# Kernel tuning notes

Hardware: AMD Instinct MI355X
Metric: run time of the kernel (lower is better)

Reference implementation:

```python
import jax, jax.numpy as jnp
import numpy as np

HIDDEN = 512
D = 2 * HIDDEN  # 1024


def setup_inputs() -> dict:
    key = jax.random.key(0)
    ks = jax.random.split(key, 7)
    B, S = 8, 2048
    scale = 1.0 / np.sqrt(D)
    return {
        "lstm_out": jax.random.normal(ks[0], (B, S, D), dtype=jnp.float32),
        "Wq": jax.random.normal(ks[1], (D, D), dtype=jnp.float32) * scale,
        "bq": jnp.zeros((D,), dtype=jnp.float32),
        "Wk": jax.random.normal(ks[2], (D, D), dtype=jnp.float32) * scale,
        "bk": jnp.zeros((D,), dtype=jnp.float32),
        "Wv": jax.random.normal(ks[3], (D, D), dtype=jnp.float32) * scale,
        "bv": jnp.zeros((D,), dtype=jnp.float32),
    }


def reference(lstm_out, Wq, bq, Wk, bk, Wv, bv):
    # Q, K, V: [B, S, D]
    Q = jnp.einsum("bsd,de->bse", lstm_out, Wq) + bq
    K = jnp.einsum("bsd,de->bse", lstm_out, Wk) + bk
    V = jnp.einsum("bsd,de->bse", lstm_out, Wv) + bv
    # NOTE: original module has no 1/sqrt(d) scaling
    scores = jnp.einsum("bqd,bkd->bqk", Q, K)  # [B, S, S]
    weights = jax.nn.softmax(scores, axis=-1)
    context = jnp.einsum("bqk,bkd->bqd", weights, V)  # [B, S, D]
    return context
```

## Files before the change

### kernel.cpp

```cpp
#include <hip/hip_runtime.h>
#include <hip/hip_bf16.h>

static constexpr int S = 2048;
static constexpr int D = 1024;
static constexpr int NB = 8;

#define LOG2E 1.4426950408889634f

typedef float    f32x4  __attribute__((ext_vector_type(4)));
typedef _Float16 f16x4  __attribute__((ext_vector_type(4)));
typedef _Float16 f16x8  __attribute__((ext_vector_type(8)));

#define CM_F32    0
#define CM_TRANSV 2
#define CM_F16    3

#define GLD16(g, l) __builtin_amdgcn_global_load_lds(                         \
    (const __attribute__((address_space(1))) void*)(g),                       \
    (__attribute__((address_space(3))) void*)(l), 16, 0, 0)

#define MFMA16(a, b, c) __builtin_amdgcn_mfma_f32_16x16x32_f16((a), (b), (c), 0, 0, 0)
#define BAR() __builtin_amdgcn_s_barrier()
#define PRIO1() __builtin_amdgcn_s_setprio(1)
#define PRIO0() __builtin_amdgcn_s_setprio(0)
#define WAIT_LGKM(n) asm volatile("s_waitcnt lgkmcnt(" #n ")" ::: "memory")
#define WAIT_VM(n)   asm volatile("s_waitcnt vmcnt(" #n ")" ::: "memory")

template <int CMODE, int BNT>
__global__ __launch_bounds__(512, 1) void bgemm256(
    const _Float16* __restrict__ Ah_, long sAz,
    const _Float16* __restrict__ Bh_, long sBz,
    int lda, int ldb,
    void* __restrict__ C1, int ldc, long sCz,
    const float* __restrict__ bias, int K)
{
    extern __shared__ char smem[];
    constexpr int NW_N  = BNT / 64;
    constexpr int NW_M  = 8 / NW_N;
    constexpr int WM    = 256 / NW_M;
    constexpr int MI    = WM / 16;
    constexpr int APLANE = 16384;
    constexpr int BPLANE = BNT * 64;
    constexpr int BOFF   = 2 * APLANE;
    constexpr int BUFSZ  = 2 * APLANE + 2 * BPLANE;

    int bx, by, bz;
    {
        const int gx = gridDim.x, gy = gridDim.y;
        const int nwg = gx * gy * gridDim.z;
        const int wg = blockIdx.x + gx * (blockIdx.y + gy * blockIdx.z);
        const int q = nwg >> 3, r = nwg & 7;
        const int xcd = wg & 7, i = wg >> 3;
        const int nid = (xcd < r) ? xcd * (q + 1) + i
                                  : r * (q + 1) + (xcd - r) * q + i;
        bx = nid % gx;
        const int tmp = nid / gx;
        by = tmp % gy;
        bz = tmp / gy;
    }

    const int t = threadIdx.x;
    const int z = bz;
    const int m0 = by * 256;
    const int n0 = bx * BNT;
    const int lane = t & 63, wid = t >> 6;
    const int wr = wid / NW_N, wc = wid % NW_N;
    const int fr = lane & 15, fq = lane >> 4;
    const int lrow = lane >> 2, lslot = lane & 3;

    const _Float16* Ahz = Ah_ + (long)z * sAz;
    const _Float16* Bhz = Bh_ + (long)z * sBz;

    auto stA = [&](int tile, int p) {
        char* lbase = smem + (tile & 1) * BUFSZ + p * APLANE;
#pragma unroll
        for (int i = 0; i < 2; ++i) {
            const int row = wid * 32 + i * 16 + lrow;
            const int chunk = lslot ^ ((row >> 1) & 3);
            const long kk = (long)tile * 64 + p * 32 + chunk * 8;
            GLD16(Ahz + (long)(m0 + row) * lda + kk,
                  lbase + (wid * 32 + i * 16) * 64);
        }
    };
    auto stB = [&](int tile, int p) {
        char* lbase = smem + (tile & 1) * BUFSZ + BOFF + p * BPLANE;
        if constexpr (BNT == 256) {
#pragma unroll
            for (int i = 0; i < 2; ++i) {
                const int row = wid * 32 + i * 16 + lrow;
                const int chunk = lslot ^ ((row >> 1) & 3);
                const long kk = (long)tile * 64 + p * 32 + chunk * 8;
                GLD16(Bhz + (long)(n0 + row) * ldb + kk,
                      lbase + (wid * 32 + i * 16) * 64);
            }
        } else {
            const int row = wid * 16 + lrow;
            const int chunk = lslot ^ ((row >> 1) & 3);
            const long kk = (long)tile * 64 + p * 32 + chunk * 8;
            GLD16(Bhz + (long)(n0 + row) * ldb + kk, lbase + (wid * 16) * 64);
        }
    };
    auto rdA = [&](int buf, int p, int mi) -> f16x8 {
        const int row = wr * WM + mi * 16 + fr;
        const int slot = fq ^ ((row >> 1) & 3);
        return *(const f16x8*)(smem + buf * BUFSZ + p * APLANE +
                               row * 64 + slot * 16);
    };
    auto rdB = [&](int buf, int p, int ni) -> f16x8 {
        const int row = wc * 64 + ni * 16 + fr;
        const int slot = fq ^ ((row >> 1) & 3);
        return *(const f16x8*)(smem + buf * BUFSZ + BOFF + p * BPLANE +
                               row * 64 + slot * 16);
    };

    f32x4 acc[MI][4] = {};
    const int ktiles = K / 64;

    {
        f16x8 b0[4], b1[4], a0[MI], a1[MI];
        auto mb = [&](f16x8 (&A)[MI], f16x8 (&B)[4]) {
#pragma unroll
            for (int mi = 0; mi < MI; ++mi)
#pragma unroll
                for (int ni = 0; ni < 4; ++ni)
                    acc[mi][ni] = MFMA16(A[mi], B[ni], acc[mi][ni]);
        };
        stA(0, 0); stB(0, 0); stA(0, 1); stB(0, 1);
        WAIT_VM(0);
        BAR();
#pragma unroll
        for (int ni = 0; ni < 4; ++ni) b0[ni] = rdB(0, 0, ni);
#pragma unroll
        for (int mi = 0; mi < MI; ++mi) a0[mi] = rdA(0, 0, mi);

        for (int tt = 0; tt < ktiles; ++tt) {
            const int buf = tt & 1;
            const bool pf = (tt + 1 < ktiles);
            if (pf) {
                stA(tt + 1, 0); stB(tt + 1, 0);
                if constexpr (BNT == 256) WAIT_VM(4); else WAIT_VM(3);
            } else {
                WAIT_VM(0);
            }
            BAR();
#pragma unroll
            for (int ni = 0; ni < 4; ++ni) b1[ni] = rdB(buf, 1, ni);
#pragma unroll
            for (int mi = 0; mi < MI; ++mi) a1[mi] = rdA(buf, 1, mi);
            if constexpr (BNT == 256) WAIT_LGKM(12); else WAIT_LGKM(8);
            PRIO1(); mb(a0, b0); PRIO0();
            BAR();
            if (pf) {
                stA(tt + 1, 1); stB(tt + 1, 1);
                if constexpr (BNT == 256) WAIT_VM(4); else WAIT_VM(3);
            }
            WAIT_LGKM(0);
            BAR();
            PRIO1(); mb(a1, b1); PRIO0();
            if (pf) {
                const int nb = buf ^ 1;
#pragma unroll
                for (int ni = 0; ni < 4; ++ni) b0[ni] = rdB(nb, 0, ni);
#pragma unroll
                for (int mi = 0; mi < MI; ++mi) a0[mi] = rdA(nb, 0, mi);
            }
        }
    }

    if constexpr (CMODE == CM_TRANSV) {
        constexpr int LDT = 544;
#pragma unroll
        for (int mi = 0; mi < MI; ++mi) {
            const int row0 = wr * WM + mi * 16 + fq * 4;
#pragma unroll
            for (int ni = 0; ni < 4; ++ni) {
                const int colp = wc * 64 + ni * 16 + fr;
                const float bv = bias[n0 + colp];
                f16x4 h;
#pragma unroll
                for (int j = 0; j < 4; ++j) h[j] = (_Float16)(acc[mi][ni][j] + bv);
                *(f16x4*)(smem + colp * LDT + row0 * 2) = h;
            }
        }
        BAR();
        const int b_ = m0 >> 11;
        const int sbase = m0 & (S - 1);
        const int l31 = lane & 31, lh = lane >> 5;
        _Float16* Vp = (_Float16*)C1;
#pragma unroll
        for (int it = 0; it < 8; ++it) {
            const int dd = wid * 16 + it * 2 + lh;
            const f16x8 v = *(const f16x8*)(smem + dd * LDT + l31 * 16);
            *(f16x8*)(Vp + ((long)(b_ * D + n0 + dd)) * S + sbase + l31 * 8) = v;
        }
    } else {
#pragma unroll
        for (int mi = 0; mi < MI; ++mi) {
            const int rbase = m0 + wr * WM + mi * 16 + fq * 4;
#pragma unroll
            for (int ni = 0; ni < 4; ++ni) {
                const int col = n0 + wc * 64 + ni * 16 + fr;
                f32x4 a = acc[mi][ni];
                if (CMODE != CM_F32) {
                    const float bv = bias[col];
#pragma unroll
                    for (int j = 0; j < 4; ++j) a[j] += bv;
                }
                if (CMODE == CM_F32) {
                    float* C = (float*)C1 + (long)z * sCz;
#pragma unroll
                    for (int j = 0; j < 4; ++j)
                        C[(long)(rbase + j) * ldc + col] = a[j];
                } else {
                    _Float16* Ch = (_Float16*)C1;
#pragma unroll
                    for (int j = 0; j < 4; ++j)
                        Ch[(long)(rbase + j) * ldc + col] = (_Float16)a[j];
                }
            }
        }
    }
}

__global__ __launch_bounds__(256) void xsplit(
    const float* __restrict__ X, _Float16* __restrict__ Xh)
{
    const long i = ((long)blockIdx.x * 256 + threadIdx.x) * 8;
    f32x4 v0 = *(const f32x4*)(X + i);
    f32x4 v1 = *(const f32x4*)(X + i + 4);
    f16x8 h;
#pragma unroll
    for (int j = 0; j < 4; ++j) { h[j] = (_Float16)v0[j]; h[4 + j] = (_Float16)v1[j]; }
    *(f16x8*)(Xh + i) = h;
}

__global__ void wsplit(const float* __restrict__ W0, const float* __restrict__ W1,
                       const float* __restrict__ W2, _Float16* __restrict__ Th)
{
    const float* W = blockIdx.z == 0 ? W0 : (blockIdx.z == 1 ? W1 : W2);
    _Float16* th = Th + (long)blockIdx.z * 1024 * 1024;
    __shared__ float tile[32][33];
    const int bx = blockIdx.x * 32, by = blockIdx.y * 32;
    const int tx = threadIdx.x, ty = threadIdx.y;
#pragma unroll
    for (int i = ty; i < 32; i += 8) tile[i][tx] = W[(long)(by + i) * 1024 + bx + tx];
    __syncthreads();
#pragma unroll
    for (int i = ty; i < 32; i += 8)
        th[(long)(bx + i) * 1024 + by + tx] = (_Float16)tile[tx][i];
}

__global__ __launch_bounds__(256) void pconv(float* __restrict__ Sb)
{
    const long row = blockIdx.x;
    float* p = Sb + row * (long)S;
    const int t = threadIdx.x;

    f32x4 x0 = *(const f32x4*)(p + t * 8);
    f32x4 x1 = *(const f32x4*)(p + t * 8 + 4);

    float m = -3.4e38f;
#pragma unroll
    for (int j = 0; j < 4; ++j) m = fmaxf(m, fmaxf(x0[j], x1[j]));
#pragma unroll
    for (int o = 32; o >= 1; o >>= 1) m = fmaxf(m, __shfl_xor(m, o));

    __shared__ float wm[4], wsum[4];
    const int wid = t >> 6, lane = t & 63;
    if (lane == 0) wm[wid] = m;
    __syncthreads();
    m = fmaxf(fmaxf(wm[0], wm[1]), fmaxf(wm[2], wm[3]));

    float e[8], ssum = 0.f;
#pragma unroll
    for (int j = 0; j < 4; ++j) {
        e[j]     = exp2f((x0[j] - m) * LOG2E);
        e[4 + j] = exp2f((x1[j] - m) * LOG2E);
        ssum += e[j] + e[4 + j];
    }
#pragma unroll
    for (int o = 32; o >= 1; o >>= 1) ssum += __shfl_xor(ssum, o);
    if (lane == 0) wsum[wid] = ssum;
    __syncthreads();
    const float invl = 1.0f / (wsum[0] + wsum[1] + wsum[2] + wsum[3]);

    f16x8 outv;
#pragma unroll
    for (int j = 0; j < 8; ++j) outv[j] = (_Float16)(e[j] * invl);
    *(f16x8*)((_Float16*)p + t * 8) = outv;
}

extern "C" void kernel_launch(void* const* d_in, const int* in_sizes, int n_in,
                              void* d_out, int out_size, void* d_ws, size_t ws_size,
                              hipStream_t stream)
{
    const float* X  = (const float*)d_in[0];
    const float* Wq = (const float*)d_in[1];
    const float* bq = (const float*)d_in[2];
    const float* Wk = (const float*)d_in[3];
    const float* bk = (const float*)d_in[4];
    const float* Wv = (const float*)d_in[5];
    const float* bv = (const float*)d_in[6];
    float* out = (float*)d_out;
    char* ws = (char*)d_ws;
    const size_t MB = 1u << 20;

    _Float16* Wh = (_Float16*)ws;
    _Float16* Qh = (_Float16*)(ws + 6 * MB);
    _Float16* Kh = (_Float16*)(ws + 38 * MB);
    _Float16* Vt = (_Float16*)(ws + 70 * MB);
    float*    Sb = (float*)(ws + 102 * MB);
    _Float16* Xh = (_Float16*)(ws + 102 * MB);

    const int LDS_256 = 131072;
    const int LDS_128 = 98304;
    (void)hipFuncSetAttribute(reinterpret_cast<const void*>(&bgemm256<CM_F16, 256>),
                        hipFuncAttributeMaxDynamicSharedMemorySize, LDS_256);
    (void)hipFuncSetAttribute(reinterpret_cast<const void*>(&bgemm256<CM_F32, 256>),
                        hipFuncAttributeMaxDynamicSharedMemorySize, LDS_256);
    (void)hipFuncSetAttribute(reinterpret_cast<const void*>(&bgemm256<CM_TRANSV, 128>),
                        hipFuncAttributeMaxDynamicSharedMemorySize, LDS_128);

    xsplit<<<dim3(8192), 256, 0, stream>>>(X, Xh);
    wsplit<<<dim3(32, 32, 3), dim3(32, 8), 0, stream>>>(Wq, Wk, Wv, Wh);

    const long MW = 1024 * 1024;
    bgemm256<CM_F16, 256><<<dim3(D / 256, 64, 1), 512, LDS_256, stream>>>(
        Xh, 0, Wh, 0, D, D, Qh, D, 0, bq, D);
    bgemm256<CM_F16, 256><<<dim3(D / 256, 64, 1), 512, LDS_256, stream>>>(
        Xh, 0, Wh + MW, 0, D, D, Kh, D, 0, bk, D);
    bgemm256<CM_TRANSV, 128><<<dim3(D / 128, 64, 1), 512, LDS_128, stream>>>(
        Xh, 0, Wh + 2 * MW, 0, D, D, Vt, 0, 0, bv, D);

    bgemm256<CM_F32, 256><<<dim3(S / 256, S / 256, NB), 512, LDS_256, stream>>>(
        Qh, (long)S * D, Kh, (long)S * D,
        D, D, Sb, S, (long)S * S, nullptr, D);
    pconv<<<dim3(NB * S), 256, 0, stream>>>(Sb);
    bgemm256<CM_F32, 256><<<dim3(D / 256, S / 256, NB), 512, LDS_256, stream>>>(
        (const _Float16*)Sb, 2L * S * S, Vt, (long)D * S,
        2 * S, S, out, D, (long)S * D, nullptr, S);
}
```

Before: 324.6 us.

## Split BNT=256 GEMM main loop into four interleaved MFMA/load phases

For the 256-wide tile variant, the k-loop now runs four half-tile MFMA phases instead of two full ones. Global-to-LDS stores and LDS fragment reads are spread between these phases, so memory traffic overlaps more with matrix math and fewer fragments are live at once. The other tile variant only has its constexpr branches simplified. The finer schedule relies on tightly tuned wait counts and adds barrier and priority toggles that could cost more than they hide.

```diff
diff --git a/kernel.cpp b/kernel.cpp
--- a/kernel.cpp
+++ b/kernel.cpp
@@ -116,7 +116,78 @@
     f32x4 acc[MI][4] = {};
     const int ktiles = K / 64;
 
-    {
+    if constexpr (BNT == 256) {
+        f16x8 b0[4], b1[4], a0[8], a1[8];
+        stA(0, 0); stB(0, 0); stA(0, 1); stB(0, 1);
+        WAIT_VM(0);
+        BAR();
+#pragma unroll
+        for (int ni = 0; ni < 4; ++ni) b0[ni] = rdB(0, 0, ni);
+#pragma unroll
+        for (int mi = 0; mi < 4; ++mi) a0[mi] = rdA(0, 0, mi);
+
+        for (int tt = 0; tt < ktiles; ++tt) {
+            const int buf = tt & 1;
+            const bool pf = (tt + 1 < ktiles);
+            if (pf) stA(tt + 1, 0);
+#pragma unroll
+            for (int mi = 0; mi < 4; ++mi) a0[4 + mi] = rdA(buf, 0, 4 + mi);
+            WAIT_LGKM(4);
+            PRIO1();
+#pragma unroll
+            for (int mi = 0; mi < 4; ++mi)
+#pragma unroll
+                for (int ni = 0; ni < 4; ++ni)
+                    acc[mi][ni] = MFMA16(a0[mi], b0[ni], acc[mi][ni]);
+            PRIO0();
+            if (pf) { stB(tt + 1, 0); WAIT_VM(4); }
+            else    { WAIT_VM(0); }
+            BAR();
+#pragma unroll
+            for (int ni = 0; ni < 4; ++ni) b1[ni] = rdB(buf, 1, ni);
+#pragma unroll
+            for (int mi = 0; mi < 4; ++mi) a1[mi] = rdA(buf, 1, mi);
+            WAIT_LGKM(8);
+            PRIO1();
+#pragma unroll
+            for (int mi = 0; mi < 4; ++mi)
+#pragma unroll
+                for (int ni = 0; ni < 4; ++ni)
+                    acc[4 + mi][ni] = MFMA16(a0[4 + mi], b0[ni], acc[4 + mi][ni]);
+            PRIO0();
+            if (pf) stA(tt + 1, 1);
+#pragma unroll
+            for (int mi = 0; mi < 4; ++mi) a1[4 + mi] = rdA(buf, 1, 4 + mi);
+            WAIT_LGKM(4);
+            PRIO1();
+#pragma unroll
+            for (int mi = 0; mi < 4; ++mi)
+#pragma unroll
+                for (int ni = 0; ni < 4; ++ni)
+                    acc[mi][ni] = MFMA16(a1[mi], b1[ni], acc[mi][ni]);
+            PRIO0();
+            if (pf) { stB(tt + 1, 1); WAIT_VM(4); }
+            else    { WAIT_VM(0); }
+            BAR();
+            if (pf) {
+                const int nb = buf ^ 1;
+#pragma unroll
+                for (int ni = 0; ni < 4; ++ni) b0[ni] = rdB(nb, 0, ni);
+#pragma unroll
+                for (int mi = 0; mi < 4; ++mi) a0[mi] = rdA(nb, 0, mi);
+                WAIT_LGKM(8);
+            } else {
+                WAIT_LGKM(0);
+            }
+            PRIO1();
+#pragma unroll
+            for (int mi = 0; mi < 4; ++mi)
+#pragma unroll
+                for (int ni = 0; ni < 4; ++ni)
+                    acc[4 + mi][ni] = MFMA16(a1[4 + mi], b1[ni], acc[4 + mi][ni]);
+            PRIO0();
+        }
+    } else {
         f16x8 b0[4], b1[4], a0[MI], a1[MI];
         auto mb = [&](f16x8 (&A)[MI], f16x8 (&B)[4]) {
 #pragma unroll
@@ -136,24 +207,17 @@
         for (int tt = 0; tt < ktiles; ++tt) {
             const int buf = tt & 1;
             const bool pf = (tt + 1 < ktiles);
-            if (pf) {
-                stA(tt + 1, 0); stB(tt + 1, 0);
-                if constexpr (BNT == 256) WAIT_VM(4); else WAIT_VM(3);
-            } else {
-                WAIT_VM(0);
-            }
+            if (pf) { stA(tt + 1, 0); stB(tt + 1, 0); WAIT_VM(3); }
+            else    { WAIT_VM(0); }
             BAR();
 #pragma unroll
             for (int ni = 0; ni < 4; ++ni) b1[ni] = rdB(buf, 1, ni);
 #pragma unroll
             for (int mi = 0; mi < MI; ++mi) a1[mi] = rdA(buf, 1, mi);
-            if constexpr (BNT == 256) WAIT_LGKM(12); else WAIT_LGKM(8);
+            WAIT_LGKM(8);
             PRIO1(); mb(a0, b0); PRIO0();
             BAR();
-            if (pf) {
-                stA(tt + 1, 1); stB(tt + 1, 1);
-                if constexpr (BNT == 256) WAIT_VM(4); else WAIT_VM(3);
-            }
+            if (pf) { stA(tt + 1, 1); stB(tt + 1, 1); WAIT_VM(3); }
             WAIT_LGKM(0);
             BAR();
             PRIO1(); mb(a1, b1); PRIO0();
```

Result: no change. 319.8 us, median of 2 (-1.5%).
